# Kernel optimization log

Hardware: AMD Instinct MI355X
Metric: run time of the kernel (lower is better)

Reference implementation:

```python
import jax, jax.numpy as jnp
import numpy as np

NUM_LEVELS = 12
BASE_RES = 16
MAX_RES = 512
LOG2_HASHMAP_SIZE = 19
HASHMAP_SIZE = 2 ** LOG2_HASHMAP_SIZE
N_POINTS = 2 ** 21  # 2,097,152 sample points


def _resolutions():
    # replicate: int(base_res * np.exp((np.log(max)-np.log(base))/(L-1)) ** i)
    growth = np.exp((np.log(MAX_RES) - np.log(BASE_RES)) / (NUM_LEVELS - 1))
    return [int(BASE_RES * growth ** i) for i in range(NUM_LEVELS)]


def setup_inputs() -> dict:
    key = jax.random.key(0)
    kx, ke = jax.random.split(key)
    x = jax.random.uniform(kx, (N_POINTS, 3), dtype=jnp.float32)  # coords in [0,1)
    embeddings = jax.random.uniform(
        ke, (NUM_LEVELS, HASHMAP_SIZE, 2), dtype=jnp.float32,
        minval=-1e-4, maxval=1e-4)
    return {"x": x, "embeddings": embeddings}


def reference(x, embeddings):
    # x: [N,3] in [0,1); embeddings: [L, T, 2]
    res = jnp.asarray(_resolutions(), dtype=x.dtype)  # [L]
    scaled = x[None, :, :] * res[:, None, None]       # [L,N,3]
    # Coords are non-negative and < 512, so int64 hash math in the torch
    # original agrees with uint32 wraparound in the low log2_hashmap_size bits.
    x0 = jnp.floor(scaled).astype(jnp.uint32)          # [L,N,3]
    primes = jnp.array([1, 2654435761, 805459861], dtype=jnp.uint32)
    t = x0 * primes                                    # [L,N,3] (mod 2^32)
    h = (t[..., 0] ^ t[..., 1] ^ t[..., 2]) % HASHMAP_SIZE  # [L,N]
    gathered = jax.vmap(lambda tab, idx: tab[idx])(embeddings, h)  # [L,N,2]
    # concat over levels along last dim -> [N, 2*L]
    return jnp.transpose(gathered, (1, 0, 2)).reshape(x.shape[0], 2 * NUM_LEVELS)
```

## Files before the change

### kernel.cpp

```cpp
#include <hip/hip_runtime.h>
#include <cmath>

typedef unsigned long long u64;
typedef __attribute__((ext_vector_type(2))) unsigned long long u64x2;

constexpr int      kLevels   = 12;
constexpr unsigned kHashSize = 1u << 19;
constexpr unsigned kHashMask = kHashSize - 1u;
constexpr int      kPoints   = 1 << 21;
constexpr int      kBlock    = 256;

constexpr int kLowLevels = 3;
constexpr int kHiLevels  = kLevels - kLowLevels;

constexpr int kILP       = 8;
constexpr int kPtsPerBlk = kBlock * kILP;
constexpr int kChunks    = kPoints / kPtsPerBlk;
constexpr int kGBlocks   = kHiLevels * kChunks;
constexpr int kXcds      = 8;
constexpr int kQLen      = kGBlocks / kXcds;

struct ResArr { float r[kLevels]; };

__global__ __launch_bounds__(kBlock) void gather_hi_kernel(
    const float* __restrict__ x,
    const u64*   __restrict__ emb,
    u64*         __restrict__ ws,
    ResArr res)
{
    const unsigned b     = blockIdx.x;
    const unsigned g     = (b % (unsigned)kXcds) * (unsigned)kQLen
                         + (b / (unsigned)kXcds);
    const unsigned li    = g / (unsigned)kChunks;
    const unsigned chunk = g - li * (unsigned)kChunks;
    const unsigned level = li + (unsigned)kLowLevels;

    float r = res.r[kLowLevels];
#pragma unroll
    for (int i = 1; i < kHiLevels; ++i)
        r = (li == (unsigned)i) ? res.r[kLowLevels + i] : r;

    const u64* __restrict__ tab = emb + (size_t)level * kHashSize;
    u64*       __restrict__ wsl = ws  + (size_t)li * kPoints;
    const unsigned base = chunk * (unsigned)kPtsPerBlk + threadIdx.x;

#pragma unroll
    for (int k = 0; k < kILP; ++k) {
        const unsigned p = base + (unsigned)(k * kBlock);
        const float px = x[p * 3u + 0u];
        const float py = x[p * 3u + 1u];
        const float pz = x[p * 3u + 2u];
        const unsigned x0 = (unsigned)floorf(px * r);
        const unsigned y0 = (unsigned)floorf(py * r);
        const unsigned z0 = (unsigned)floorf(pz * r);
        const unsigned h  = (x0 ^ (y0 * 2654435761u) ^ (z0 * 805459861u)) & kHashMask;
        const u64 e = tab[h];
        __builtin_nontemporal_store(e, wsl + p);
    }
}

__global__ __launch_bounds__(kBlock) void assemble_kernel(
    const float* __restrict__ x,
    const u64*   __restrict__ emb,
    const u64*   __restrict__ ws,
    u64x2*       __restrict__ out,
    ResArr res)
{
    __shared__ u64 lds[kBlock][kLevels + 1];
    const unsigned t    = threadIdx.x;
    const unsigned base = blockIdx.x * (unsigned)kBlock;
    const unsigned p    = base + t;

    const float px = x[p * 3u + 0u];
    const float py = x[p * 3u + 1u];
    const float pz = x[p * 3u + 2u];

#pragma unroll
    for (int l = 0; l < kLowLevels; ++l) {
        const float r = res.r[l];
        const unsigned x0 = (unsigned)floorf(px * r);
        const unsigned y0 = (unsigned)floorf(py * r);
        const unsigned z0 = (unsigned)floorf(pz * r);
        const unsigned h  = (x0 ^ (y0 * 2654435761u) ^ (z0 * 805459861u)) & kHashMask;
        lds[t][l] = emb[(size_t)l * kHashSize + h];
    }
#pragma unroll
    for (int li = 0; li < kHiLevels; ++li) {
        lds[t][kLowLevels + li] =
            __builtin_nontemporal_load(ws + (size_t)li * kPoints + p);
    }
    __syncthreads();

#pragma unroll
    for (int j = 0; j < 6; ++j) {
        const unsigned el = (unsigned)(j * kBlock) + t;
        const unsigned p2 = el / 6u;
        const unsigned s2 = el - p2 * 6u;
        u64x2 o;
        o.x = lds[p2][2u * s2 + 0u];
        o.y = lds[p2][2u * s2 + 1u];
        __builtin_nontemporal_store(o, out + (size_t)base * 6u + el);
    }
}

__global__ __launch_bounds__(kBlock) void direct_kernel(
    const float* __restrict__ x,
    const u64*   __restrict__ emb,
    u64*         __restrict__ out,
    ResArr res)
{
    unsigned tid = blockIdx.x * (unsigned)kBlock + threadIdx.x;
    unsigned n   = tid / (unsigned)kLevels;
    unsigned l   = tid - n * (unsigned)kLevels;
    float r = res.r[0];
#pragma unroll
    for (int i = 1; i < kLevels; ++i) r = (l == (unsigned)i) ? res.r[i] : r;
    float px = x[n * 3u], py = x[n * 3u + 1u], pz = x[n * 3u + 2u];
    unsigned x0 = (unsigned)floorf(px * r);
    unsigned y0 = (unsigned)floorf(py * r);
    unsigned z0 = (unsigned)floorf(pz * r);
    unsigned h  = (x0 ^ (y0 * 2654435761u) ^ (z0 * 805459861u)) & kHashMask;
    __builtin_nontemporal_store(emb[l * kHashSize + h], out + tid);
}

extern "C" void kernel_launch(void* const* d_in, const int* in_sizes, int n_in,
                              void* d_out, int out_size, void* d_ws, size_t ws_size,
                              hipStream_t stream) {
    const float* x   = (const float*)d_in[0];
    const u64*   emb = (const u64*)d_in[1];

    ResArr res;
    const double growth = std::exp((std::log(512.0) - std::log(16.0)) / 11.0);
    for (int i = 0; i < kLevels; ++i)
        res.r[i] = (float)(int)(16.0 * std::pow(growth, (double)i));

    const size_t ws_needed = (size_t)kHiLevels * kPoints * sizeof(u64);

    if (ws_size >= ws_needed) {
        hipLaunchKernelGGL(gather_hi_kernel, dim3(kGBlocks), dim3(kBlock), 0, stream,
                           x, emb, (u64*)d_ws, res);
        hipLaunchKernelGGL(assemble_kernel, dim3(kPoints / kBlock), dim3(kBlock), 0, stream,
                           x, emb, (const u64*)d_ws, (u64x2*)d_out, res);
    } else {
        const int total = kPoints * kLevels;
        hipLaunchKernelGGL(direct_kernel, dim3(total / kBlock), dim3(kBlock), 0, stream,
                           x, emb, (u64*)d_out, res);
    }
}
```

Before: 221.0 us.

## Split points into halves and overlap second-half gather with first-half assembly

Splits the work into two point halves. A gather kernel handles the first half, then a mixed kernel interleaves second-half gather blocks with first-half assemble blocks, and a final kernel assembles the second half. This is meant to overlap the random-access gather traffic with the streaming output writes instead of running the two phases back to back. The gather ILP also doubles to 16, with all hash loads issued before any stores and an asm barrier holding them in registers, which raises register pressure and adds a third kernel launch.

```diff
diff --git a/kernel.cpp b/kernel.cpp
--- a/kernel.cpp
+++ b/kernel.cpp
@@ -8,31 +8,35 @@
 constexpr unsigned kHashSize = 1u << 19;
 constexpr unsigned kHashMask = kHashSize - 1u;
 constexpr int      kPoints   = 1 << 21;
+constexpr int      kHalf     = kPoints / 2;
 constexpr int      kBlock    = 256;
 
 constexpr int kLowLevels = 3;
 constexpr int kHiLevels  = kLevels - kLowLevels;
 
-constexpr int kILP       = 8;
+constexpr int kILP       = 16;
 constexpr int kPtsPerBlk = kBlock * kILP;
-constexpr int kChunks    = kPoints / kPtsPerBlk;
-constexpr int kGBlocks   = kHiLevels * kChunks;
+constexpr int kChunksH   = kHalf / kPtsPerBlk;
+constexpr int kGBlocksH  = kHiLevels * kChunksH;
 constexpr int kXcds      = 8;
-constexpr int kQLen      = kGBlocks / kXcds;
+constexpr int kQLenH     = kGBlocksH / kXcds;
+
+constexpr int kABlocksH  = kHalf / kBlock;
+
+constexpr int kInterleaved = 2 * kGBlocksH;
+constexpr int kMixBlocks   = kInterleaved + (kABlocksH - kGBlocksH);
 
 struct ResArr { float r[kLevels]; };
 
-__global__ __launch_bounds__(kBlock) void gather_hi_kernel(
-    const float* __restrict__ x,
-    const u64*   __restrict__ emb,
-    u64*         __restrict__ ws,
-    ResArr res)
-{
-    const unsigned b     = blockIdx.x;
-    const unsigned g     = (b % (unsigned)kXcds) * (unsigned)kQLen
-                         + (b / (unsigned)kXcds);
-    const unsigned li    = g / (unsigned)kChunks;
-    const unsigned chunk = g - li * (unsigned)kChunks;
+__device__ __forceinline__ void gather_work(
+    unsigned g, unsigned half_base,
+    const float* __restrict__ x, const u64* __restrict__ emb,
+    u64* __restrict__ ws, const ResArr& res)
+{
+    const unsigned gq    = (g % (unsigned)kXcds) * (unsigned)kQLenH
+                         + (g / (unsigned)kXcds);
+    const unsigned li    = gq / (unsigned)kChunksH;
+    const unsigned chunk = gq - li * (unsigned)kChunksH;
     const unsigned level = li + (unsigned)kLowLevels;
 
     float r = res.r[kLowLevels];
@@ -42,34 +46,44 @@
 
     const u64* __restrict__ tab = emb + (size_t)level * kHashSize;
     u64*       __restrict__ wsl = ws  + (size_t)li * kPoints;
-    const unsigned base = chunk * (unsigned)kPtsPerBlk + threadIdx.x;
-
+    const unsigned base = half_base + chunk * (unsigned)kPtsPerBlk + threadIdx.x;
+
+    unsigned h[kILP];
 #pragma unroll
     for (int k = 0; k < kILP; ++k) {
         const unsigned p = base + (unsigned)(k * kBlock);
         const float px = x[p * 3u + 0u];
         const float py = x[p * 3u + 1u];
         const float pz = x[p * 3u + 2u];
-        const unsigned x0 = (unsigned)floorf(px * r);
-        const unsigned y0 = (unsigned)floorf(py * r);
-        const unsigned z0 = (unsigned)floorf(pz * r);
-        const unsigned h  = (x0 ^ (y0 * 2654435761u) ^ (z0 * 805459861u)) & kHashMask;
-        const u64 e = tab[h];
-        __builtin_nontemporal_store(e, wsl + p);
-    }
-}
-
-__global__ __launch_bounds__(kBlock) void assemble_kernel(
-    const float* __restrict__ x,
-    const u64*   __restrict__ emb,
-    const u64*   __restrict__ ws,
-    u64x2*       __restrict__ out,
-    ResArr res)
-{
-    __shared__ u64 lds[kBlock][kLevels + 1];
-    const unsigned t    = threadIdx.x;
-    const unsigned base = blockIdx.x * (unsigned)kBlock;
-    const unsigned p    = base + t;
+        h[k] = ((unsigned)floorf(px * r)
+              ^ ((unsigned)floorf(py * r) * 2654435761u)
+              ^ ((unsigned)floorf(pz * r) * 805459861u)) & kHashMask;
+    }
+
+    u64 e[kILP];
+#pragma unroll
+    for (int k = 0; k < kILP; ++k)
+        e[k] = tab[h[k]];
+
+    asm volatile("" ::
+        "v"(e[0]),  "v"(e[1]),  "v"(e[2]),  "v"(e[3]),
+        "v"(e[4]),  "v"(e[5]),  "v"(e[6]),  "v"(e[7]),
+        "v"(e[8]),  "v"(e[9]),  "v"(e[10]), "v"(e[11]),
+        "v"(e[12]), "v"(e[13]), "v"(e[14]), "v"(e[15]));
+
+#pragma unroll
+    for (int k = 0; k < kILP; ++k)
+        __builtin_nontemporal_store(e[k], wsl + base + (unsigned)(k * kBlock));
+}
+
+__device__ __forceinline__ void assemble_work(
+    unsigned pbase,
+    const float* __restrict__ x, const u64* __restrict__ emb,
+    const u64* __restrict__ ws, u64x2* __restrict__ out,
+    const ResArr& res, u64 (*lds)[kLevels + 1])
+{
+    const unsigned t = threadIdx.x;
+    const unsigned p = pbase + t;
 
     const float px = x[p * 3u + 0u];
     const float py = x[p * 3u + 1u];
@@ -99,8 +113,46 @@
         u64x2 o;
         o.x = lds[p2][2u * s2 + 0u];
         o.y = lds[p2][2u * s2 + 1u];
-        __builtin_nontemporal_store(o, out + (size_t)base * 6u + el);
-    }
+        __builtin_nontemporal_store(o, out + (size_t)pbase * 6u + el);
+    }
+}
+
+__global__ __launch_bounds__(kBlock) void gather_a_kernel(
+    const float* __restrict__ x, const u64* __restrict__ emb,
+    u64* __restrict__ ws, ResArr res)
+{
+    gather_work(blockIdx.x, 0u, x, emb, ws, res);
+}
+
+__global__ __launch_bounds__(kBlock) void mix_kernel(
+    const float* __restrict__ x, const u64* __restrict__ emb,
+    u64* __restrict__ ws, u64x2* __restrict__ out, ResArr res)
+{
+    __shared__ u64 lds[kBlock][kLevels + 1];
+    const unsigned bid = blockIdx.x;
+    if (bid < (unsigned)kInterleaved) {
+        const unsigned grp  = bid >> 4;
+        const unsigned slot = bid & 15u;
+        if (slot < 8u) {
+            const unsigned g = grp * 8u + slot;
+            gather_work(g, (unsigned)kHalf, x, emb, ws, res);
+        } else {
+            const unsigned a = grp * 8u + (slot - 8u);
+            assemble_work(a * (unsigned)kBlock, x, emb, ws, out, res, lds);
+        }
+    } else {
+        const unsigned a = (unsigned)kGBlocksH + (bid - (unsigned)kInterleaved);
+        assemble_work(a * (unsigned)kBlock, x, emb, ws, out, res, lds);
+    }
+}
+
+__global__ __launch_bounds__(kBlock) void assemble_b_kernel(
+    const float* __restrict__ x, const u64* __restrict__ emb,
+    const u64* __restrict__ ws, u64x2* __restrict__ out, ResArr res)
+{
+    __shared__ u64 lds[kBlock][kLevels + 1];
+    assemble_work((unsigned)kHalf + blockIdx.x * (unsigned)kBlock,
+                  x, emb, ws, out, res, lds);
 }
 
 __global__ __launch_bounds__(kBlock) void direct_kernel(
@@ -137,9 +189,11 @@
     const size_t ws_needed = (size_t)kHiLevels * kPoints * sizeof(u64);
 
     if (ws_size >= ws_needed) {
-        hipLaunchKernelGGL(gather_hi_kernel, dim3(kGBlocks), dim3(kBlock), 0, stream,
+        hipLaunchKernelGGL(gather_a_kernel, dim3(kGBlocksH), dim3(kBlock), 0, stream,
                            x, emb, (u64*)d_ws, res);
-        hipLaunchKernelGGL(assemble_kernel, dim3(kPoints / kBlock), dim3(kBlock), 0, stream,
+        hipLaunchKernelGGL(mix_kernel, dim3(kMixBlocks), dim3(kBlock), 0, stream,
+                           x, emb, (u64*)d_ws, (u64x2*)d_out, res);
+        hipLaunchKernelGGL(assemble_b_kernel, dim3(kABlocksH), dim3(kBlock), 0, stream,
                            x, emb, (const u64*)d_ws, (u64x2*)d_out, res);
     } else {
         const int total = kPoints * kLevels;
```

Result: slower. 257.9 us (+16.7%).
